# Performance work log

Measured on AMD Instinct MI355X. Metric: run time of the kernel, lower is better.

## Reference

```python
import jax, jax.numpy as jnp
import numpy as np

B, C, I, E = 2048, 256, 9, 10


def _contraction(U_list, W_list, x, y):
    """Recursive symmetric contraction for one output irrep.
    U_list/W_list ordered [U1, U2, U3] (correlation 1..3).
    x: [b, c, i], y: [b, e]. Returns flattened [b, c * m].
    """
    U3, W3 = U_list[-1], W_list[-1]
    # main: '...ik,ekc,bci,be->bc...'
    out = jnp.einsum('...ik,ekc,bci,be->bc...', U3, W3, x, y)
    for corr in range(len(U_list) - 2, -1, -1):
        U, W = U_list[corr], W_list[corr]
        # weighting: '...k,ekc,be->bc...'
        c_tensor = jnp.einsum('...k,ekc,be->bc...', U, W, y) + out
        # contract: 'bc...i,bci->bc...'
        out = jnp.einsum('bc...i,bci->bc...', c_tensor, x)
    return out.reshape(out.shape[0], -1)


def setup_inputs() -> dict:
    key = jax.random.key(0)
    ks = jax.random.split(key, 14)
    inp = {
        'x': jax.random.normal(ks[0], (B, C, I), jnp.float32),
        'y': jax.random.uniform(ks[1], (B, E), jnp.float32),
        'U1_s': jax.random.normal(ks[2], (I, 1), jnp.float32),
        'U2_s': jax.random.normal(ks[3], (I, I, 3), jnp.float32),
        'U3_s': jax.random.normal(ks[4], (I, I, I, 23), jnp.float32),
        'U1_v': jax.random.normal(ks[5], (3, I, 1), jnp.float32),
        'U2_v': jax.random.normal(ks[6], (3, I, I, 4), jnp.float32),
        'U3_v': jax.random.normal(ks[7], (3, I, I, I, 30), jnp.float32),
        'W1_s': jax.random.normal(ks[8], (E, 1, C), jnp.float32),
        'W2_s': jax.random.normal(ks[9], (E, 3, C), jnp.float32) / 3.0,
        'W3_s': jax.random.normal(ks[10], (E, 23, C), jnp.float32) / 23.0,
        'W1_v': jax.random.normal(ks[11], (E, 1, C), jnp.float32),
        'W2_v': jax.random.normal(ks[12], (E, 4, C), jnp.float32) / 4.0,
        'W3_v': jax.random.normal(ks[13], (E, 30, C), jnp.float32) / 30.0,
    }
    return inp


def reference(x, y, U1_s, U2_s, U3_s, U1_v, U2_v, U3_v,
              W1_s, W2_s, W3_s, W1_v, W2_v, W3_v):
    out_s = _contraction([U1_s, U2_s, U3_s], [W1_s, W2_s, W3_s], x, y)  # [b, c]
    out_v = _contraction([U1_v, U2_v, U3_v], [W1_v, W2_v, W3_v], x, y)  # [b, c*3]
    return jnp.concatenate([out_s, out_v], axis=-1)  # [b, 4c]
```

## Files before the change

### kernel.cpp

```cpp
#include <hip/hip_runtime.h>
#include <hip/hip_bf16.h>


#define NB 2048
#define NC 256
#define NI 9
#define NE 10

#define N_TRI 165
#define N_PAIR 45
#define BT 8

#define T3N (N_TRI * NE * NC)
#define T2N (N_PAIR * NE * NC)
#define T1N (NI * NE * NC)

__global__ __launch_bounds__(256) void sc_prep(
    const float* __restrict__ U1_s, const float* __restrict__ U2_s,
    const float* __restrict__ U3_s, const float* __restrict__ U1_v,
    const float* __restrict__ U2_v, const float* __restrict__ U3_v,
    const float* __restrict__ W1_s, const float* __restrict__ W2_s,
    const float* __restrict__ W3_s, const float* __restrict__ W1_v,
    const float* __restrict__ W2_v, const float* __restrict__ W3_v,
    float* __restrict__ ws)
{
    const int m = blockIdx.x;
    const int e = blockIdx.y;
    const int tid = threadIdx.x;
    float4* __restrict__ T3 = (float4*)ws;
    float4* __restrict__ T2 = T3 + T3N;
    float4* __restrict__ T1 = T2 + T2N;

    __shared__ float sym[128];

    if (m < N_TRI) {
        if (tid < 113) {
            int ii = 0, jj = 0, kk = 0, cnt = 0;
            for (int i = 0; i < NI; i++)
                for (int j = i; j < NI; j++)
                    for (int k = j; k < NI; k++) {
                        if (cnt == m) { ii = i; jj = j; kk = k; }
                        cnt++;
                    }
            int P[6][3]; int np;
            if (ii == jj && jj == kk) {
                np = 1;
                P[0][0] = ii; P[0][1] = ii; P[0][2] = ii;
            } else if (ii == jj) {
                np = 3;
                P[0][0] = ii; P[0][1] = ii; P[0][2] = kk;
                P[1][0] = ii; P[1][1] = kk; P[1][2] = ii;
                P[2][0] = kk; P[2][1] = ii; P[2][2] = ii;
            } else if (jj == kk) {
                np = 3;
                P[0][0] = ii; P[0][1] = jj; P[0][2] = jj;
                P[1][0] = jj; P[1][1] = ii; P[1][2] = jj;
                P[2][0] = jj; P[2][1] = jj; P[2][2] = ii;
            } else {
                np = 6;
                P[0][0] = ii; P[0][1] = jj; P[0][2] = kk;
                P[1][0] = ii; P[1][1] = kk; P[1][2] = jj;
                P[2][0] = jj; P[2][1] = ii; P[2][2] = kk;
                P[3][0] = jj; P[3][1] = kk; P[3][2] = ii;
                P[4][0] = kk; P[4][1] = ii; P[4][2] = jj;
                P[5][0] = kk; P[5][1] = jj; P[5][2] = ii;
            }
            float s = 0.f;
            if (tid < 23) {
                for (int p = 0; p < np; p++)
                    s += U3_s[((P[p][0] * NI + P[p][1]) * NI + P[p][2]) * 23 + tid];
            } else {
                int a = (tid - 23) / 30, t = (tid - 23) % 30;
                for (int p = 0; p < np; p++)
                    s += U3_v[(((a * NI + P[p][0]) * NI + P[p][1]) * NI + P[p][2]) * 30 + t];
            }
            sym[tid] = s;
        }
        __syncthreads();
        const int c = tid;
        float s = 0.f, v0 = 0.f, v1 = 0.f, v2 = 0.f;
        #pragma unroll
        for (int t = 0; t < 23; t++)
            s = fmaf(sym[t], W3_s[(e * 23 + t) * NC + c], s);
        #pragma unroll
        for (int t = 0; t < 30; t++) {
            float wv = W3_v[(e * 30 + t) * NC + c];
            v0 = fmaf(sym[23 + t], wv, v0);
            v1 = fmaf(sym[53 + t], wv, v1);
            v2 = fmaf(sym[83 + t], wv, v2);
        }
        T3[(m * NE + e) * NC + c] = make_float4(s, v0, v1, v2);
    } else if (m < N_TRI + N_PAIR) {
        const int mm = m - N_TRI;
        if (tid < 15) {
            int ii = 0, jj = 0, cnt = 0;
            for (int i = 0; i < NI; i++)
                for (int j = i; j < NI; j++) {
                    if (cnt == mm) { ii = i; jj = j; }
                    cnt++;
                }
            float s;
            if (tid < 3) {
                s = U2_s[(ii * NI + jj) * 3 + tid];
                if (ii != jj) s += U2_s[(jj * NI + ii) * 3 + tid];
            } else {
                int a = (tid - 3) / 4, t = (tid - 3) % 4;
                s = U2_v[((a * NI + ii) * NI + jj) * 4 + t];
                if (ii != jj) s += U2_v[((a * NI + jj) * NI + ii) * 4 + t];
            }
            sym[tid] = s;
        }
        __syncthreads();
        const int c = tid;
        float s = 0.f, v0 = 0.f, v1 = 0.f, v2 = 0.f;
        #pragma unroll
        for (int t = 0; t < 3; t++)
            s = fmaf(sym[t], W2_s[(e * 3 + t) * NC + c], s);
        #pragma unroll
        for (int t = 0; t < 4; t++) {
            float wv = W2_v[(e * 4 + t) * NC + c];
            v0 = fmaf(sym[3 + t],  wv, v0);
            v1 = fmaf(sym[7 + t],  wv, v1);
            v2 = fmaf(sym[11 + t], wv, v2);
        }
        T2[(mm * NE + e) * NC + c] = make_float4(s, v0, v1, v2);
    } else {
        const int i = m - N_TRI - N_PAIR;
        const int c = tid;
        float w1s = W1_s[e * NC + c], w1v = W1_v[e * NC + c];
        T1[(i * NE + e) * NC + c] = make_float4(
            U1_s[i] * w1s,
            U1_v[0 * NI + i] * w1v,
            U1_v[1 * NI + i] * w1v,
            U1_v[2 * NI + i] * w1v);
    }
}

__device__ __forceinline__ void tri_advance(int& i, int& j, int& k) {
    k++;
    if (k == NI) { j++; if (j == NI) { i++; j = i; } k = j; }
}

#define ROW_FMA(BUF)                                              \
    {                                                             \
        _Pragma("unroll")                                         \
        for (int e = 0; e < NE; e++) {                            \
            const float4 t = BUF[e];                              \
            _Pragma("unroll")                                     \
            for (int n = 0; n < BT; n++) {                        \
                const float p = w[e][n] * phi[n];                 \
                acc[n][0] = fmaf(p, t.x, acc[n][0]);              \
                acc[n][1] = fmaf(p, t.y, acc[n][1]);              \
                acc[n][2] = fmaf(p, t.z, acc[n][2]);              \
                acc[n][3] = fmaf(p, t.w, acc[n][3]);              \
            }                                                     \
        }                                                         \
    }

template <int M0, int M1, int I0, int J0, int K0>
__device__ __forceinline__ void do_triples(
    const float4* __restrict__ T3, int c, const float* __restrict__ xb,
    const float (&w)[NE][BT], float (&acc)[BT][4])
{
    float4 bufA[NE], bufB[NE];
    #pragma unroll
    for (int e = 0; e < NE; e++) bufA[e] = T3[(M0 * NE + e) * NC + c];
    int i = I0, j = J0, k = K0;
    for (int m = M0; m + 1 < M1; m += 2) {
        #pragma unroll
        for (int e = 0; e < NE; e++) bufB[e] = T3[((m + 1) * NE + e) * NC + c];
        {
            float phi[BT];
            #pragma unroll
            for (int n = 0; n < BT; n++)
                phi[n] = xb[(i * BT + n) * 64] * xb[(j * BT + n) * 64]
                       * xb[(k * BT + n) * 64];
            ROW_FMA(bufA)
        }
        tri_advance(i, j, k);
        const int mp = (m + 2 < M1) ? m + 2 : M1 - 1;
        #pragma unroll
        for (int e = 0; e < NE; e++) bufA[e] = T3[(mp * NE + e) * NC + c];
        {
            float phi[BT];
            #pragma unroll
            for (int n = 0; n < BT; n++)
                phi[n] = xb[(i * BT + n) * 64] * xb[(j * BT + n) * 64]
                       * xb[(k * BT + n) * 64];
            ROW_FMA(bufB)
        }
        tri_advance(i, j, k);
    }
    if ((M1 - M0) & 1) {
        float phi[BT];
        #pragma unroll
        for (int n = 0; n < BT; n++)
            phi[n] = xb[(i * BT + n) * 64] * xb[(j * BT + n) * 64]
                   * xb[(k * BT + n) * 64];
        ROW_FMA(bufA)
    }
}

__global__ __launch_bounds__(256) void sc_main(
    const float* __restrict__ x, const float* __restrict__ y,
    const float* __restrict__ ws, float* __restrict__ out)
{
    const int tid = threadIdx.x;
    const int tx  = tid & 63;
    const int wv  = __builtin_amdgcn_readfirstlane(tid >> 6);
    const int bid = blockIdx.x;
    const int xcd    = bid & 7;
    const int c_tile = xcd >> 1;
    const int b_tile = ((bid >> 3) << 1) | (xcd & 1);
    const int c0 = c_tile << 6;
    const int c  = c0 + tx;
    const int b0 = b_tile << 3;

    __shared__ float xs[NI][BT][64];
    __shared__ float red[BT][4][64];

    #pragma unroll
    for (int p = 0; p < 2; p++) {
        const int pair = tid + p * 256;
        const int n = pair >> 6, cc = pair & 63;
        const float* xp = x + ((size_t)(b0 + n) * NC + c0 + cc) * NI;
        #pragma unroll
        for (int i = 0; i < NI; i++) xs[i][n][cc] = xp[i];
    }
    __syncthreads();
    const float* xb = &xs[0][0][tx];

    float w[NE][BT];
    #pragma unroll
    for (int n = 0; n < BT; n++)
        #pragma unroll
        for (int e = 0; e < NE; e++) w[e][n] = y[(b0 + n) * NE + e];

    float acc[BT][4];
    #pragma unroll
    for (int n = 0; n < BT; n++)
        #pragma unroll
        for (int h = 0; h < 4; h++) acc[n][h] = 0.f;

    const float4* __restrict__ T3 = (const float4*)ws;
    const float4* __restrict__ T2 = T3 + T3N;
    const float4* __restrict__ T1 = T2 + T2N;

    if (wv == 0) {
        do_triples<0, 55, 0, 0, 0>(T3, c, xb, w, acc);
    } else if (wv == 1) {
        do_triples<55, 110, 1, 2, 4>(T3, c, xb, w, acc);
    } else if (wv == 2) {
        do_triples<110, N_TRI, 3, 3, 4>(T3, c, xb, w, acc);
    } else {
        {
            float4 bufA[NE], bufB[NE];
            #pragma unroll
            for (int e = 0; e < NE; e++) bufA[e] = T2[e * NC + c];
            int i = 0, j = 0;
            for (int m = 0; m + 1 < N_PAIR; m += 2) {
                #pragma unroll
                for (int e = 0; e < NE; e++) bufB[e] = T2[((m + 1) * NE + e) * NC + c];
                {
                    float phi[BT];
                    #pragma unroll
                    for (int n = 0; n < BT; n++)
                        phi[n] = xb[(i * BT + n) * 64] * xb[(j * BT + n) * 64];
                    ROW_FMA(bufA)
                }
                j++; if (j == NI) { i++; j = i; }
                const int mp = (m + 2 < N_PAIR) ? m + 2 : N_PAIR - 1;
                #pragma unroll
                for (int e = 0; e < NE; e++) bufA[e] = T2[(mp * NE + e) * NC + c];
                {
                    float phi[BT];
                    #pragma unroll
                    for (int n = 0; n < BT; n++)
                        phi[n] = xb[(i * BT + n) * 64] * xb[(j * BT + n) * 64];
                    ROW_FMA(bufB)
                }
                j++; if (j == NI) { i++; j = i; }
            }
            {
                float phi[BT];
                #pragma unroll
                for (int n = 0; n < BT; n++)
                    phi[n] = xb[(i * BT + n) * 64] * xb[(j * BT + n) * 64];
                ROW_FMA(bufA)
            }
        }
        for (int i = 0; i < NI; i++) {
            float4 tc[NE];
            #pragma unroll
            for (int e = 0; e < NE; e++) tc[e] = T1[(i * NE + e) * NC + c];
            float phi[BT];
            #pragma unroll
            for (int n = 0; n < BT; n++) phi[n] = xb[(i * BT + n) * 64];
            ROW_FMA(tc)
        }
    }

    if (wv == 0) {
        #pragma unroll
        for (int n = 0; n < BT; n++)
            #pragma unroll
            for (int h = 0; h < 4; h++) red[n][h][tx] = acc[n][h];
    }
    __syncthreads();
    if (wv == 1) {
        #pragma unroll
        for (int n = 0; n < BT; n++)
            #pragma unroll
            for (int h = 0; h < 4; h++) acc[n][h] += red[n][h][tx];
    }
    __syncthreads();
    if (wv == 1) {
        #pragma unroll
        for (int n = 0; n < BT; n++)
            #pragma unroll
            for (int h = 0; h < 4; h++) red[n][h][tx] = acc[n][h];
    }
    __syncthreads();
    if (wv == 2) {
        #pragma unroll
        for (int n = 0; n < BT; n++)
            #pragma unroll
            for (int h = 0; h < 4; h++) acc[n][h] += red[n][h][tx];
    }
    __syncthreads();
    if (wv == 2) {
        #pragma unroll
        for (int n = 0; n < BT; n++)
            #pragma unroll
            for (int h = 0; h < 4; h++) red[n][h][tx] = acc[n][h];
    }
    __syncthreads();
    if (wv == 3) {
        #pragma unroll
        for (int n = 0; n < BT; n++) {
            float* ob = out + (size_t)(b0 + n) * (4 * NC);
            ob[c]              = acc[n][0] + red[n][0][tx];
            ob[NC + 3 * c + 0] = acc[n][1] + red[n][1][tx];
            ob[NC + 3 * c + 1] = acc[n][2] + red[n][2][tx];
            ob[NC + 3 * c + 2] = acc[n][3] + red[n][3][tx];
        }
    }
}

extern "C" void kernel_launch(void* const* d_in, const int* in_sizes, int n_in,
                              void* d_out, int out_size, void* d_ws, size_t ws_size,
                              hipStream_t stream) {
    const float* x    = (const float*)d_in[0];
    const float* y    = (const float*)d_in[1];
    const float* U1_s = (const float*)d_in[2];
    const float* U2_s = (const float*)d_in[3];
    const float* U3_s = (const float*)d_in[4];
    const float* U1_v = (const float*)d_in[5];
    const float* U2_v = (const float*)d_in[6];
    const float* U3_v = (const float*)d_in[7];
    const float* W1_s = (const float*)d_in[8];
    const float* W2_s = (const float*)d_in[9];
    const float* W3_s = (const float*)d_in[10];
    const float* W1_v = (const float*)d_in[11];
    const float* W2_v = (const float*)d_in[12];
    const float* W3_v = (const float*)d_in[13];
    float* out = (float*)d_out;
    float* ws  = (float*)d_ws;

    sc_prep<<<dim3(N_TRI + N_PAIR + NI, NE), 256, 0, stream>>>(
        U1_s, U2_s, U3_s, U1_v, U2_v, U3_v,
        W1_s, W2_s, W3_s, W1_v, W2_v, W3_v, ws);
    sc_main<<<1024, 256, 0, stream>>>(x, y, ws, out);
}
```

Measured before the change: 265.1 us.

## Split per-block work across eight waves with tree reduction

Doubles the block size to 512 threads so eight wavefronts share the triple, pair and single contractions for each (b-tile, c-tile). Each wave takes about half the rows it handled before, and the partial sums are combined with a pairwise tree reduction in shared memory instead of a serial chain. The aim is more latency hiding per CU and a shorter critical path per block. In exchange it uses more shared memory for the reduction buffers, adds barriers, and may lower register budget or occupancy per wave under launch_bounds(512).

```diff
diff --git a/kernel.cpp b/kernel.cpp
--- a/kernel.cpp
+++ b/kernel.cpp
@@ -136,11 +136,6 @@
     }
 }
 
-__device__ __forceinline__ void tri_advance(int& i, int& j, int& k) {
-    k++;
-    if (k == NI) { j++; if (j == NI) { i++; j = i; } k = j; }
-}
-
 #define ROW_FMA(BUF)                                              \
     {                                                             \
         _Pragma("unroll")                                         \
@@ -177,7 +172,7 @@
                        * xb[(k * BT + n) * 64];
             ROW_FMA(bufA)
         }
-        tri_advance(i, j, k);
+        k++; if (k == NI) { j++; if (j == NI) { i++; j = i; } k = j; }
         const int mp = (m + 2 < M1) ? m + 2 : M1 - 1;
         #pragma unroll
         for (int e = 0; e < NE; e++) bufA[e] = T3[(mp * NE + e) * NC + c];
@@ -189,7 +184,7 @@
                        * xb[(k * BT + n) * 64];
             ROW_FMA(bufB)
         }
-        tri_advance(i, j, k);
+        k++; if (k == NI) { j++; if (j == NI) { i++; j = i; } k = j; }
     }
     if ((M1 - M0) & 1) {
         float phi[BT];
@@ -201,7 +196,63 @@
     }
 }
 
-__global__ __launch_bounds__(256) void sc_main(
+template <int M0, int M1, int I0, int J0>
+__device__ __forceinline__ void do_pairs(
+    const float4* __restrict__ T2, int c, const float* __restrict__ xb,
+    const float (&w)[NE][BT], float (&acc)[BT][4])
+{
+    float4 bufA[NE], bufB[NE];
+    #pragma unroll
+    for (int e = 0; e < NE; e++) bufA[e] = T2[(M0 * NE + e) * NC + c];
+    int i = I0, j = J0;
+    for (int m = M0; m + 1 < M1; m += 2) {
+        #pragma unroll
+        for (int e = 0; e < NE; e++) bufB[e] = T2[((m + 1) * NE + e) * NC + c];
+        {
+            float phi[BT];
+            #pragma unroll
+            for (int n = 0; n < BT; n++)
+                phi[n] = xb[(i * BT + n) * 64] * xb[(j * BT + n) * 64];
+            ROW_FMA(bufA)
+        }
+        j++; if (j == NI) { i++; j = i; }
+        const int mp = (m + 2 < M1) ? m + 2 : M1 - 1;
+        #pragma unroll
+        for (int e = 0; e < NE; e++) bufA[e] = T2[(mp * NE + e) * NC + c];
+        {
+            float phi[BT];
+            #pragma unroll
+            for (int n = 0; n < BT; n++)
+                phi[n] = xb[(i * BT + n) * 64] * xb[(j * BT + n) * 64];
+            ROW_FMA(bufB)
+        }
+        j++; if (j == NI) { i++; j = i; }
+    }
+    if ((M1 - M0) & 1) {
+        float phi[BT];
+        #pragma unroll
+        for (int n = 0; n < BT; n++)
+            phi[n] = xb[(i * BT + n) * 64] * xb[(j * BT + n) * 64];
+        ROW_FMA(bufA)
+    }
+}
+
+__device__ __forceinline__ void do_singles(
+    const float4* __restrict__ T1, int c, const float* __restrict__ xb,
+    const float (&w)[NE][BT], float (&acc)[BT][4])
+{
+    for (int i = 0; i < NI; i++) {
+        float4 tc[NE];
+        #pragma unroll
+        for (int e = 0; e < NE; e++) tc[e] = T1[(i * NE + e) * NC + c];
+        float phi[BT];
+        #pragma unroll
+        for (int n = 0; n < BT; n++) phi[n] = xb[(i * BT + n) * 64];
+        ROW_FMA(tc)
+    }
+}
+
+__global__ __launch_bounds__(512) void sc_main(
     const float* __restrict__ x, const float* __restrict__ y,
     const float* __restrict__ ws, float* __restrict__ out)
 {
@@ -217,12 +268,10 @@
     const int b0 = b_tile << 3;
 
     __shared__ float xs[NI][BT][64];
-    __shared__ float red[BT][4][64];
-
-    #pragma unroll
-    for (int p = 0; p < 2; p++) {
-        const int pair = tid + p * 256;
-        const int n = pair >> 6, cc = pair & 63;
+    __shared__ float red[4][BT][4][64];
+
+    {
+        const int n = tid >> 6, cc = tid & 63;
         const float* xp = x + ((size_t)(b0 + n) * NC + c0 + cc) * NI;
         #pragma unroll
         for (int i = 0; i < NI; i++) xs[i][n][cc] = xp[i];
@@ -246,103 +295,65 @@
     const float4* __restrict__ T2 = T3 + T3N;
     const float4* __restrict__ T1 = T2 + T2N;
 
-    if (wv == 0) {
-        do_triples<0, 55, 0, 0, 0>(T3, c, xb, w, acc);
-    } else if (wv == 1) {
-        do_triples<55, 110, 1, 2, 4>(T3, c, xb, w, acc);
-    } else if (wv == 2) {
-        do_triples<110, N_TRI, 3, 3, 4>(T3, c, xb, w, acc);
-    } else {
-        {
-            float4 bufA[NE], bufB[NE];
-            #pragma unroll
-            for (int e = 0; e < NE; e++) bufA[e] = T2[e * NC + c];
-            int i = 0, j = 0;
-            for (int m = 0; m + 1 < N_PAIR; m += 2) {
-                #pragma unroll
-                for (int e = 0; e < NE; e++) bufB[e] = T2[((m + 1) * NE + e) * NC + c];
-                {
-                    float phi[BT];
-                    #pragma unroll
-                    for (int n = 0; n < BT; n++)
-                        phi[n] = xb[(i * BT + n) * 64] * xb[(j * BT + n) * 64];
-                    ROW_FMA(bufA)
-                }
-                j++; if (j == NI) { i++; j = i; }
-                const int mp = (m + 2 < N_PAIR) ? m + 2 : N_PAIR - 1;
-                #pragma unroll
-                for (int e = 0; e < NE; e++) bufA[e] = T2[(mp * NE + e) * NC + c];
-                {
-                    float phi[BT];
-                    #pragma unroll
-                    for (int n = 0; n < BT; n++)
-                        phi[n] = xb[(i * BT + n) * 64] * xb[(j * BT + n) * 64];
-                    ROW_FMA(bufB)
-                }
-                j++; if (j == NI) { i++; j = i; }
-            }
-            {
-                float phi[BT];
-                #pragma unroll
-                for (int n = 0; n < BT; n++)
-                    phi[n] = xb[(i * BT + n) * 64] * xb[(j * BT + n) * 64];
-                ROW_FMA(bufA)
-            }
-        }
-        for (int i = 0; i < NI; i++) {
-            float4 tc[NE];
-            #pragma unroll
-            for (int e = 0; e < NE; e++) tc[e] = T1[(i * NE + e) * NC + c];
-            float phi[BT];
-            #pragma unroll
-            for (int n = 0; n < BT; n++) phi[n] = xb[(i * BT + n) * 64];
-            ROW_FMA(tc)
-        }
-    }
-
-    if (wv == 0) {
-        #pragma unroll
-        for (int n = 0; n < BT; n++)
-            #pragma unroll
-            for (int h = 0; h < 4; h++) red[n][h][tx] = acc[n][h];
-    }
-    __syncthreads();
-    if (wv == 1) {
-        #pragma unroll
-        for (int n = 0; n < BT; n++)
-            #pragma unroll
-            for (int h = 0; h < 4; h++) acc[n][h] += red[n][h][tx];
-    }
-    __syncthreads();
-    if (wv == 1) {
-        #pragma unroll
-        for (int n = 0; n < BT; n++)
-            #pragma unroll
-            for (int h = 0; h < 4; h++) red[n][h][tx] = acc[n][h];
-    }
-    __syncthreads();
-    if (wv == 2) {
-        #pragma unroll
-        for (int n = 0; n < BT; n++)
-            #pragma unroll
-            for (int h = 0; h < 4; h++) acc[n][h] += red[n][h][tx];
-    }
-    __syncthreads();
-    if (wv == 2) {
-        #pragma unroll
-        for (int n = 0; n < BT; n++)
-            #pragma unroll
-            for (int h = 0; h < 4; h++) red[n][h][tx] = acc[n][h];
+    if      (wv == 0) do_triples<0,   28, 0, 0, 0>(T3, c, xb, w, acc);
+    else if (wv == 1) do_triples<28,  55, 0, 3, 7>(T3, c, xb, w, acc);
+    else if (wv == 2) do_triples<55,  83, 1, 2, 4>(T3, c, xb, w, acc);
+    else if (wv == 3) do_triples<83, 110, 2, 2, 4>(T3, c, xb, w, acc);
+    else if (wv == 4) do_triples<110, 138, 3, 3, 4>(T3, c, xb, w, acc);
+    else if (wv == 5) do_triples<138, 165, 4, 5, 8>(T3, c, xb, w, acc);
+    else if (wv == 6) do_pairs<0, 27, 0, 0>(T2, c, xb, w, acc);
+    else {
+        do_pairs<27, N_PAIR, 3, 6>(T2, c, xb, w, acc);
+        do_singles(T1, c, xb, w, acc);
+    }
+
+    if (wv == 0 || wv == 2 || wv == 4 || wv == 6) {
+        float (*r)[4][64] = red[wv >> 1];
+        #pragma unroll
+        for (int n = 0; n < BT; n++)
+            #pragma unroll
+            for (int h = 0; h < 4; h++) r[n][h][tx] = acc[n][h];
+    }
+    __syncthreads();
+    if (wv == 1 || wv == 3 || wv == 5 || wv == 7) {
+        float (*r)[4][64] = red[wv >> 1];
+        #pragma unroll
+        for (int n = 0; n < BT; n++)
+            #pragma unroll
+            for (int h = 0; h < 4; h++) acc[n][h] += r[n][h][tx];
+    }
+    __syncthreads();
+    if (wv == 1 || wv == 5) {
+        float (*r)[4][64] = red[wv >> 2];
+        #pragma unroll
+        for (int n = 0; n < BT; n++)
+            #pragma unroll
+            for (int h = 0; h < 4; h++) r[n][h][tx] = acc[n][h];
+    }
+    __syncthreads();
+    if (wv == 3 || wv == 7) {
+        float (*r)[4][64] = red[wv >> 2];
+        #pragma unroll
+        for (int n = 0; n < BT; n++)
+            #pragma unroll
+            for (int h = 0; h < 4; h++) acc[n][h] += r[n][h][tx];
     }
     __syncthreads();
     if (wv == 3) {
+        #pragma unroll
+        for (int n = 0; n < BT; n++)
+            #pragma unroll
+            for (int h = 0; h < 4; h++) red[0][n][h][tx] = acc[n][h];
+    }
+    __syncthreads();
+    if (wv == 7) {
         #pragma unroll
         for (int n = 0; n < BT; n++) {
             float* ob = out + (size_t)(b0 + n) * (4 * NC);
-            ob[c]              = acc[n][0] + red[n][0][tx];
-            ob[NC + 3 * c + 0] = acc[n][1] + red[n][1][tx];
-            ob[NC + 3 * c + 1] = acc[n][2] + red[n][2][tx];
-            ob[NC + 3 * c + 2] = acc[n][3] + red[n][3][tx];
+            ob[c]              = acc[n][0] + red[0][n][0][tx];
+            ob[NC + 3 * c + 0] = acc[n][1] + red[0][n][1][tx];
+            ob[NC + 3 * c + 1] = acc[n][2] + red[0][n][2][tx];
+            ob[NC + 3 * c + 2] = acc[n][3] + red[0][n][3][tx];
         }
     }
 }
@@ -370,5 +381,5 @@
     sc_prep<<<dim3(N_TRI + N_PAIR + NI, NE), 256, 0, stream>>>(
         U1_s, U2_s, U3_s, U1_v, U2_v, U3_v,
         W1_s, W2_s, W3_s, W1_v, W2_v, W3_v, ws);
-    sc_main<<<1024, 256, 0, stream>>>(x, y, ws, out);
-}
+    sc_main<<<1024, 512, 0, stream>>>(x, y, ws, out);
+}
```

Measured after the change: 338.5 us. 1.28x slower.
